# Kernel tuning notes

Hardware: AMD Instinct MI355X
Metric: run time of the kernel (lower is better)

## Reference

```python
import jax, jax.numpy as jnp
import numpy as np

C = 320          # channels
N = 65536        # flattened samples per channel (batch * H * W)
FT = (1, 3, 3, 3, 1)  # (1,) + filters + (1,)
INIT_SCALE = 10.0


def setup_inputs() -> dict:
    key = jax.random.key(0)
    ks = jax.random.split(key, 8)
    inp = {"inputs": jax.random.normal(ks[0], (C, 1, N), dtype=jnp.float32)}
    scale = INIT_SCALE ** (1.0 / (len(FT) - 1))
    for i in range(len(FT) - 1):
        init = float(np.log(np.expm1(1.0 / scale / FT[i + 1])))
        inp[f"M{i}"] = jnp.full((C, FT[i + 1], FT[i]), init, dtype=jnp.float32)
        inp[f"b{i}"] = jax.random.uniform(ks[1 + i], (C, FT[i + 1], 1),
                                           minval=-0.5, maxval=0.5,
                                           dtype=jnp.float32)
        if i < len(FT) - 2:
            inp[f"f{i}"] = jnp.zeros((C, FT[i + 1], 1), dtype=jnp.float32)
    inp["stop_gradient"] = 0
    return inp


def reference(inputs, M0, M1, M2, M3, b0, b1, b2, b3, f0, f1, f2, stop_gradient):
    Ms = [M0, M1, M2, M3]
    bs = [b0, b1, b2, b3]
    fs = [f0, f1, f2]
    sg = (lambda x: jax.lax.stop_gradient(x)) if stop_gradient else (lambda x: x)
    logits = inputs  # (C, 1, N)
    for i in range(len(FT) - 1):
        m = jax.nn.softplus(sg(Ms[i]))                 # (C, f_{i+1}, f_i)
        logits = jnp.einsum('cij,cjn->cin', m, logits) + sg(bs[i])
        if i < len(FT) - 2:
            logits = logits + jnp.tanh(sg(fs[i])) * jnp.tanh(logits)
    return logits  # (C, 1, N)
```

## Files before the change

### kernel.cpp

```cpp
#include <hip/hip_runtime.h>
#include <cmath>


#define CCH 320
#define NN 65536
#define BLK 256
#define BLOCKS_PER_CH 8
#define WS_STRIDE 64

typedef float vfloat4 __attribute__((ext_vector_type(4)));


__device__ __forceinline__ float softplus_fast(float x) {
    return fmaxf(x, 0.0f) + __logf(1.0f + __expf(-fabsf(x)));
}
__device__ __forceinline__ float tanh_fast(float x) {
    return 1.0f - 2.0f / (__expf(2.0f * x) + 1.0f);
}

__global__ __launch_bounds__(BLK) void cdf_precompute_kernel(
    const float* __restrict__ M0, const float* __restrict__ b0, const float* __restrict__ f0,
    const float* __restrict__ M1, const float* __restrict__ b1, const float* __restrict__ f1,
    const float* __restrict__ M2, const float* __restrict__ b2, const float* __restrict__ f2,
    const float* __restrict__ M3, const float* __restrict__ b3,
    float* __restrict__ ws)
{
    const int c = blockIdx.x * BLK + threadIdx.x;
    if (c >= CCH) return;
    float* w = ws + (size_t)c * WS_STRIDE;

    float m0[3], B0[3], t0[3], m1[9], B1[3], t1[3], m2[9], B2[3], t2[3], m3[3];
#pragma unroll
    for (int i = 0; i < 3; ++i) {
        m0[i] = softplus_fast(M0[c * 3 + i]);
        B0[i] = b0[c * 3 + i];
        t0[i] = tanh_fast(f0[c * 3 + i]);
        B1[i] = b1[c * 3 + i];
        t1[i] = tanh_fast(f1[c * 3 + i]);
        B2[i] = b2[c * 3 + i];
        t2[i] = tanh_fast(f2[c * 3 + i]);
        m3[i] = softplus_fast(M3[c * 3 + i]);
    }
#pragma unroll
    for (int i = 0; i < 9; ++i) {
        m1[i] = softplus_fast(M1[c * 9 + i]);
        m2[i] = softplus_fast(M2[c * 9 + i]);
    }
    const float B3 = b3[c];

    const bool gated = t0[0] != 0.f || t0[1] != 0.f || t0[2] != 0.f ||
                       t1[0] != 0.f || t1[1] != 0.f || t1[2] != 0.f ||
                       t2[0] != 0.f || t2[1] != 0.f || t2[2] != 0.f;

    double w1[3], u1[3], w2[3], u2[3];
#pragma unroll
    for (int i = 0; i < 3; ++i) {
        w1[i] = (double)m1[i*3+0]*m0[0] + (double)m1[i*3+1]*m0[1] + (double)m1[i*3+2]*m0[2];
        u1[i] = (double)m1[i*3+0]*B0[0] + (double)m1[i*3+1]*B0[1] + (double)m1[i*3+2]*B0[2] + B1[i];
    }
#pragma unroll
    for (int i = 0; i < 3; ++i) {
        w2[i] = (double)m2[i*3+0]*w1[0] + (double)m2[i*3+1]*w1[1] + (double)m2[i*3+2]*w1[2];
        u2[i] = (double)m2[i*3+0]*u1[0] + (double)m2[i*3+1]*u1[1] + (double)m2[i*3+2]*u1[2] + B2[i];
    }
    const double a = (double)m3[0]*w2[0] + (double)m3[1]*w2[1] + (double)m3[2]*w2[2];
    const double b = (double)m3[0]*u2[0] + (double)m3[1]*u2[1] + (double)m3[2]*u2[2] + B3;

    w[0] = (float)a;
    w[1] = (float)b;
    w[2] = gated ? 1.0f : 0.0f;
#pragma unroll
    for (int i = 0; i < 3; ++i) {
        w[4 + i]  = m0[i];  w[7 + i]  = B0[i];  w[10 + i] = t0[i];
        w[22 + i] = B1[i];  w[25 + i] = t1[i];
        w[37 + i] = B2[i];  w[40 + i] = t2[i];  w[43 + i] = m3[i];
    }
#pragma unroll
    for (int i = 0; i < 9; ++i) { w[13 + i] = m1[i]; w[28 + i] = m2[i]; }
    w[46] = B3;
}

__global__ __launch_bounds__(BLK) void cdf_stream_kernel(
    const float* __restrict__ in, const float* __restrict__ ws,
    float* __restrict__ out)
{
    const int c = blockIdx.y;
    const float* __restrict__ w = ws + (size_t)c * WS_STRIDE;

    const vfloat4* __restrict__ inv  = reinterpret_cast<const vfloat4*>(in + (size_t)c * NN);
    vfloat4* __restrict__       outv = reinterpret_cast<vfloat4*>(out + (size_t)c * NN);

    const int tid    = blockIdx.x * BLK + threadIdx.x;
    const int stride = BLOCKS_PER_CH * BLK;
    constexpr int ITERS = (NN / 4) / (BLOCKS_PER_CH * BLK);

    if (__builtin_expect(w[2] == 0.0f, 1)) {
        const float a = w[0], b = w[1];
#pragma unroll
        for (int it = 0; it < ITERS; ++it) {
            const int i = tid + it * stride;
            const vfloat4 x = inv[i];
            vfloat4 r;
            r.x = fmaf(a, x.x, b);
            r.y = fmaf(a, x.y, b);
            r.z = fmaf(a, x.z, b);
            r.w = fmaf(a, x.w, b);
            outv[i] = r;
        }
        return;
    }

    float m0[3], B0[3], t0[3], m1[9], B1[3], t1[3], m2[9], B2[3], t2[3], m3[3];
#pragma unroll
    for (int i = 0; i < 3; ++i) {
        m0[i] = w[4 + i];  B0[i] = w[7 + i];  t0[i] = w[10 + i];
        B1[i] = w[22 + i]; t1[i] = w[25 + i];
        B2[i] = w[37 + i]; t2[i] = w[40 + i]; m3[i] = w[43 + i];
    }
#pragma unroll
    for (int i = 0; i < 9; ++i) { m1[i] = w[13 + i]; m2[i] = w[28 + i]; }
    const float B3 = w[46];

#pragma unroll
    for (int it = 0; it < ITERS; ++it) {
        const int i = tid + it * stride;
        const vfloat4 x = inv[i];
        float r[4] = {x.x, x.y, x.z, x.w};
#pragma unroll
        for (int k = 0; k < 4; ++k) {
            const float v = r[k];
            float h0[3], h1[3], h2[3];
#pragma unroll
            for (int j = 0; j < 3; ++j) {
                h0[j] = fmaf(m0[j], v, B0[j]);
                h0[j] = fmaf(t0[j], tanh_fast(h0[j]), h0[j]);
            }
#pragma unroll
            for (int j = 0; j < 3; ++j) {
                h1[j] = fmaf(m1[j*3+0], h0[0],
                        fmaf(m1[j*3+1], h0[1],
                        fmaf(m1[j*3+2], h0[2], B1[j])));
                h1[j] = fmaf(t1[j], tanh_fast(h1[j]), h1[j]);
            }
#pragma unroll
            for (int j = 0; j < 3; ++j) {
                h2[j] = fmaf(m2[j*3+0], h1[0],
                        fmaf(m2[j*3+1], h1[1],
                        fmaf(m2[j*3+2], h1[2], B2[j])));
                h2[j] = fmaf(t2[j], tanh_fast(h2[j]), h2[j]);
            }
            r[k] = fmaf(m3[0], h2[0], fmaf(m3[1], h2[1], fmaf(m3[2], h2[2], B3)));
        }
        vfloat4 o; o.x = r[0]; o.y = r[1]; o.z = r[2]; o.w = r[3];
        outv[i] = o;
    }
}

extern "C" void kernel_launch(void* const* d_in, const int* in_sizes, int n_in,
                              void* d_out, int out_size, void* d_ws, size_t ws_size,
                              hipStream_t stream) {
    const float* in = (const float*)d_in[0];
    const float* M0 = (const float*)d_in[1];
    const float* b0 = (const float*)d_in[2];
    const float* f0 = (const float*)d_in[3];
    const float* M1 = (const float*)d_in[4];
    const float* b1 = (const float*)d_in[5];
    const float* f1 = (const float*)d_in[6];
    const float* M2 = (const float*)d_in[7];
    const float* b2 = (const float*)d_in[8];
    const float* f2 = (const float*)d_in[9];
    const float* M3 = (const float*)d_in[10];
    const float* b3 = (const float*)d_in[11];
    float* out = (float*)d_out;
    float* ws  = (float*)d_ws;

    cdf_precompute_kernel<<<dim3((CCH + BLK - 1) / BLK), BLK, 0, stream>>>(
        M0, b0, f0, M1, b1, f1, M2, b2, f2, M3, b3, ws);

    dim3 grid(BLOCKS_PER_CH, CCH);
    cdf_stream_kernel<<<grid, BLK, 0, stream>>>(in, ws, out);
}
```

Before: 174.6 us.

## Split stream kernel into two half-channel launches with nontemporal access for second half

Replaces the per-channel grid-stride loop, where each thread handled eight float4s, with one float4 per thread over a flat 1D grid. The work is split into two launches of 160 channels each. The second launch uses nontemporal loads and stores on the fast path, so the first half's data may stay in the cache hierarchy while the second half streams past it. The cost is an extra kernel launch and far more blocks, and the benefit depends on how the cache behaves across consecutive launches.

```diff
diff --git a/kernel.cpp b/kernel.cpp
--- a/kernel.cpp
+++ b/kernel.cpp
@@ -5,7 +5,9 @@
 #define CCH 320
 #define NN 65536
 #define BLK 256
-#define BLOCKS_PER_CH 8
+#define NV 16384
+#define BPC 64
+#define HC 160
 #define WS_STRIDE 64
 
 typedef float vfloat4 __attribute__((ext_vector_type(4)));
@@ -32,19 +34,19 @@
     float m0[3], B0[3], t0[3], m1[9], B1[3], t1[3], m2[9], B2[3], t2[3], m3[3];
 #pragma unroll
     for (int i = 0; i < 3; ++i) {
-        m0[i] = softplus_fast(M0[c * 3 + i]);
-        B0[i] = b0[c * 3 + i];
-        t0[i] = tanh_fast(f0[c * 3 + i]);
-        B1[i] = b1[c * 3 + i];
-        t1[i] = tanh_fast(f1[c * 3 + i]);
-        B2[i] = b2[c * 3 + i];
-        t2[i] = tanh_fast(f2[c * 3 + i]);
-        m3[i] = softplus_fast(M3[c * 3 + i]);
+        m0[i] = softplus_fast(M0[c*3+i]);
+        B0[i] = b0[c*3+i];
+        t0[i] = tanh_fast(f0[c*3+i]);
+        B1[i] = b1[c*3+i];
+        t1[i] = tanh_fast(f1[c*3+i]);
+        B2[i] = b2[c*3+i];
+        t2[i] = tanh_fast(f2[c*3+i]);
+        m3[i] = softplus_fast(M3[c*3+i]);
     }
 #pragma unroll
     for (int i = 0; i < 9; ++i) {
-        m1[i] = softplus_fast(M1[c * 9 + i]);
-        m2[i] = softplus_fast(M2[c * 9 + i]);
+        m1[i] = softplus_fast(M1[c*9+i]);
+        m2[i] = softplus_fast(M2[c*9+i]);
     }
     const float B3 = b3[c];
 
@@ -63,11 +65,8 @@
         w2[i] = (double)m2[i*3+0]*w1[0] + (double)m2[i*3+1]*w1[1] + (double)m2[i*3+2]*w1[2];
         u2[i] = (double)m2[i*3+0]*u1[0] + (double)m2[i*3+1]*u1[1] + (double)m2[i*3+2]*u1[2] + B2[i];
     }
-    const double a = (double)m3[0]*w2[0] + (double)m3[1]*w2[1] + (double)m3[2]*w2[2];
-    const double b = (double)m3[0]*u2[0] + (double)m3[1]*u2[1] + (double)m3[2]*u2[2] + B3;
-
-    w[0] = (float)a;
-    w[1] = (float)b;
+    w[0] = (float)((double)m3[0]*w2[0] + (double)m3[1]*w2[1] + (double)m3[2]*w2[2]);
+    w[1] = (float)((double)m3[0]*u2[0] + (double)m3[1]*u2[1] + (double)m3[2]*u2[2] + B3);
     w[2] = gated ? 1.0f : 0.0f;
 #pragma unroll
     for (int i = 0; i < 3; ++i) {
@@ -80,33 +79,29 @@
     w[46] = B3;
 }
 
+template <bool NT>
 __global__ __launch_bounds__(BLK) void cdf_stream_kernel(
     const float* __restrict__ in, const float* __restrict__ ws,
-    float* __restrict__ out)
+    float* __restrict__ out, int ch0)
 {
-    const int c = blockIdx.y;
+    const int c = ch0 + (blockIdx.x >> 6);
+    const int idx = (size_t)c * NV + (blockIdx.x & 63) * BLK + threadIdx.x;
+
+    const vfloat4* __restrict__ inv  = reinterpret_cast<const vfloat4*>(in);
+    vfloat4* __restrict__       outv = reinterpret_cast<vfloat4*>(out);
     const float* __restrict__ w = ws + (size_t)c * WS_STRIDE;
 
-    const vfloat4* __restrict__ inv  = reinterpret_cast<const vfloat4*>(in + (size_t)c * NN);
-    vfloat4* __restrict__       outv = reinterpret_cast<vfloat4*>(out + (size_t)c * NN);
-
-    const int tid    = blockIdx.x * BLK + threadIdx.x;
-    const int stride = BLOCKS_PER_CH * BLK;
-    constexpr int ITERS = (NN / 4) / (BLOCKS_PER_CH * BLK);
+    const vfloat4 x = NT ? __builtin_nontemporal_load(&inv[idx]) : inv[idx];
 
     if (__builtin_expect(w[2] == 0.0f, 1)) {
         const float a = w[0], b = w[1];
-#pragma unroll
-        for (int it = 0; it < ITERS; ++it) {
-            const int i = tid + it * stride;
-            const vfloat4 x = inv[i];
-            vfloat4 r;
-            r.x = fmaf(a, x.x, b);
-            r.y = fmaf(a, x.y, b);
-            r.z = fmaf(a, x.z, b);
-            r.w = fmaf(a, x.w, b);
-            outv[i] = r;
-        }
+        vfloat4 r;
+        r.x = fmaf(a, x.x, b);
+        r.y = fmaf(a, x.y, b);
+        r.z = fmaf(a, x.z, b);
+        r.w = fmaf(a, x.w, b);
+        if (NT) __builtin_nontemporal_store(r, &outv[idx]);
+        else    outv[idx] = r;
         return;
     }
 
@@ -121,39 +116,34 @@
     for (int i = 0; i < 9; ++i) { m1[i] = w[13 + i]; m2[i] = w[28 + i]; }
     const float B3 = w[46];
 
+    float r[4] = {x.x, x.y, x.z, x.w};
 #pragma unroll
-    for (int it = 0; it < ITERS; ++it) {
-        const int i = tid + it * stride;
-        const vfloat4 x = inv[i];
-        float r[4] = {x.x, x.y, x.z, x.w};
+    for (int k = 0; k < 4; ++k) {
+        const float v = r[k];
+        float h0[3], h1[3], h2[3];
 #pragma unroll
-        for (int k = 0; k < 4; ++k) {
-            const float v = r[k];
-            float h0[3], h1[3], h2[3];
+        for (int j = 0; j < 3; ++j) {
+            h0[j] = fmaf(m0[j], v, B0[j]);
+            h0[j] = fmaf(t0[j], tanh_fast(h0[j]), h0[j]);
+        }
 #pragma unroll
-            for (int j = 0; j < 3; ++j) {
-                h0[j] = fmaf(m0[j], v, B0[j]);
-                h0[j] = fmaf(t0[j], tanh_fast(h0[j]), h0[j]);
-            }
+        for (int j = 0; j < 3; ++j) {
+            h1[j] = fmaf(m1[j*3+0], h0[0],
+                    fmaf(m1[j*3+1], h0[1],
+                    fmaf(m1[j*3+2], h0[2], B1[j])));
+            h1[j] = fmaf(t1[j], tanh_fast(h1[j]), h1[j]);
+        }
 #pragma unroll
-            for (int j = 0; j < 3; ++j) {
-                h1[j] = fmaf(m1[j*3+0], h0[0],
-                        fmaf(m1[j*3+1], h0[1],
-                        fmaf(m1[j*3+2], h0[2], B1[j])));
-                h1[j] = fmaf(t1[j], tanh_fast(h1[j]), h1[j]);
-            }
-#pragma unroll
-            for (int j = 0; j < 3; ++j) {
-                h2[j] = fmaf(m2[j*3+0], h1[0],
-                        fmaf(m2[j*3+1], h1[1],
-                        fmaf(m2[j*3+2], h1[2], B2[j])));
-                h2[j] = fmaf(t2[j], tanh_fast(h2[j]), h2[j]);
-            }
-            r[k] = fmaf(m3[0], h2[0], fmaf(m3[1], h2[1], fmaf(m3[2], h2[2], B3)));
+        for (int j = 0; j < 3; ++j) {
+            h2[j] = fmaf(m2[j*3+0], h1[0],
+                    fmaf(m2[j*3+1], h1[1],
+                    fmaf(m2[j*3+2], h1[2], B2[j])));
+            h2[j] = fmaf(t2[j], tanh_fast(h2[j]), h2[j]);
         }
-        vfloat4 o; o.x = r[0]; o.y = r[1]; o.z = r[2]; o.w = r[3];
-        outv[i] = o;
+        r[k] = fmaf(m3[0], h2[0], fmaf(m3[1], h2[1], fmaf(m3[2], h2[2], B3)));
     }
+    vfloat4 o; o.x = r[0]; o.y = r[1]; o.z = r[2]; o.w = r[3];
+    outv[idx] = o;
 }
 
 extern "C" void kernel_launch(void* const* d_in, const int* in_sizes, int n_in,
@@ -177,6 +167,6 @@
     cdf_precompute_kernel<<<dim3((CCH + BLK - 1) / BLK), BLK, 0, stream>>>(
         M0, b0, f0, M1, b1, f1, M2, b2, f2, M3, b3, ws);
 
-    dim3 grid(BLOCKS_PER_CH, CCH);
-    cdf_stream_kernel<<<grid, BLK, 0, stream>>>(in, ws, out);
+    cdf_stream_kernel<false><<<dim3(HC * BPC), BLK, 0, stream>>>(in, ws, out, 0);
+    cdf_stream_kernel<true><<<dim3(HC * BPC), BLK, 0, stream>>>(in, ws, out, HC);
 }
```

After: 173.8 us. Within noise of the previous version (-0.5%).
